# Optimization experiments

Hardware: AMD Instinct MI355X
Metric: run time of the kernel (lower is better)

Reference implementation:

```python
import jax, jax.numpy as jnp
import numpy as np

JACCARD_THRESH = 0.5
NEGPOS_RATIO = 3
V0, V1 = 0.1, 0.2  # SSD encoding variances


def setup_inputs() -> dict:
    key = jax.random.key(0)
    k1, k2, k3, k4, k5, k6, k7 = jax.random.split(key, 7)
    B, P, C, O = 128, 8732, 21, 16
    loc_data = jax.random.normal(k1, (B, P, 4), dtype=jnp.float32)
    conf_data = jax.random.normal(k2, (B, P, C), dtype=jnp.float32)
    # default boxes in center form (cx, cy, w, h), all in [0,1]
    cxcy = jax.random.uniform(k3, (P, 2), minval=0.05, maxval=0.95)
    wh = jax.random.uniform(k4, (P, 2), minval=0.05, maxval=0.6)
    dbox_list = jnp.concatenate([cxcy, wh], axis=1).astype(jnp.float32)
    # ground-truth boxes in corner form with guaranteed positive extent
    tl = jax.random.uniform(k5, (B, O, 2), minval=0.0, maxval=0.6)
    sz = jax.random.uniform(k6, (B, O, 2), minval=0.05, maxval=0.35)
    labels = jax.random.randint(k7, (B, O, 1), 0, C - 1).astype(jnp.float32)
    targets = jnp.concatenate([tl, tl + sz, labels], axis=2)
    return {"loc_data": loc_data, "conf_data": conf_data,
            "dbox_list": dbox_list, "targets": targets}


def _match_one(truths, labels, dbox):
    """SSD match for one image. truths:[O,4] corner, labels:[O], dbox:[P,4] center."""
    pf = jnp.concatenate([dbox[:, :2] - dbox[:, 2:] * 0.5,
                          dbox[:, :2] + dbox[:, 2:] * 0.5], axis=1)  # point form [P,4]
    lt = jnp.maximum(truths[:, None, :2], pf[None, :, :2])
    rb = jnp.minimum(truths[:, None, 2:], pf[None, :, 2:])
    whi = jnp.clip(rb - lt, 0.0)
    inter = whi[..., 0] * whi[..., 1]                                # [O,P]
    area_t = (truths[:, 2] - truths[:, 0]) * (truths[:, 3] - truths[:, 1])
    area_p = dbox[:, 2] * dbox[:, 3]
    ov = inter / (area_t[:, None] + area_p[None, :] - inter)         # jaccard [O,P]
    best_prior_idx = jnp.argmax(ov, axis=1)                          # [O]
    bto = jnp.max(ov, axis=0)                                        # [P]
    bti = jnp.argmax(ov, axis=0)                                     # [P]
    bto = bto.at[best_prior_idx].set(2.0)
    O = truths.shape[0]
    bti = jax.lax.fori_loop(0, O, lambda j, b: b.at[best_prior_idx[j]].set(j), bti)
    matched = truths[bti]                                            # [P,4]
    conf = labels[bti].astype(jnp.int32) + 1
    conf = jnp.where(bto < JACCARD_THRESH, 0, conf)
    g_cxcy = ((matched[:, :2] + matched[:, 2:]) * 0.5 - dbox[:, :2]) / (V0 * dbox[:, 2:])
    g_wh = jnp.log((matched[:, 2:] - matched[:, :2]) / dbox[:, 2:]) / V1
    return jnp.concatenate([g_cxcy, g_wh], axis=1), conf


def reference(loc_data, conf_data, dbox_list, targets):
    B, P, C = conf_data.shape
    loc_t, conf_t = jax.vmap(_match_one, in_axes=(0, 0, None))(
        targets[..., :4], targets[..., 4], dbox_list)
    pos = conf_t > 0                                                  # [B,P]
    # smooth L1 (beta=1), summed over positives
    ad = jnp.abs(loc_data - loc_t)
    sl1 = jnp.where(ad < 1.0, 0.5 * ad * ad, ad - 0.5)
    loss_l = jnp.sum(jnp.where(pos[..., None], sl1, 0.0))
    # per-prior cross entropy
    logp = jax.nn.log_softmax(conf_data, axis=-1)
    ce = -jnp.take_along_axis(logp, conf_t[..., None], axis=-1)[..., 0]  # [B,P]
    # hard negative mining via double argsort (rank in descending order)
    ce_neg = jnp.where(pos, 0.0, ce)
    loss_idx = jnp.argsort(-ce_neg, axis=1)
    idx_rank = jnp.argsort(loss_idx, axis=1)
    num_pos = jnp.sum(pos, axis=1, keepdims=True)
    num_neg = jnp.minimum(num_pos * NEGPOS_RATIO, P)
    neg = idx_rank < num_neg
    sel = pos | neg
    loss_c = jnp.sum(jnp.where(sel, ce, 0.0))
    N = jnp.sum(num_pos).astype(loc_data.dtype)
    return jnp.stack([loss_l / N, loss_c / N])
```

## Files before the change

### kernel.cpp

```cpp
#include <hip/hip_runtime.h>
#include <cstddef>

#define Bn 128
#define Pn 8732
#define Cn 21
#define On 16
#define MAGIC 0x13579BDFu

__device__ __forceinline__ void argmax_combine(float& v, int& p, float v2, int p2) {
  if (v2 > v || (v2 == v && p2 < p)) { v = v2; p = p2; }
}

__device__ __forceinline__ float sl1_enc(float4 lv, float4 d,
                                         float t0, float t1, float t2, float t3) {
  float g0 = ((t0 + t2) * 0.5f - d.x) / (0.1f * d.z);
  float g1 = ((t1 + t3) * 0.5f - d.y) / (0.1f * d.w);
  float g2 = __logf((t2 - t0) / d.z) / 0.2f;
  float g3 = __logf((t3 - t1) / d.w) / 0.2f;
  float r = 0.f, a;
  a = fabsf(lv.x - g0); r += (a < 1.f) ? 0.5f * a * a : a - 0.5f;
  a = fabsf(lv.y - g1); r += (a < 1.f) ? 0.5f * a * a : a - 0.5f;
  a = fabsf(lv.z - g2); r += (a < 1.f) ? 0.5f * a * a : a - 0.5f;
  a = fabsf(lv.w - g3); r += (a < 1.f) ? 0.5f * a * a : a - 0.5f;
  return r;
}

__global__ __launch_bounds__(256) void stream_kernel(
    const float* __restrict__ conf, const float* __restrict__ dbox,
    const float* __restrict__ targets,
    float* __restrict__ ce0, unsigned char* __restrict__ pack,
    unsigned long long* __restrict__ keys) {
  const int wb = threadIdx.x >> 6, lane = threadIdx.x & 63;
  const int wave_g = blockIdx.x * 4 + wb;
  const int b = wave_g & 127;
  const int cg = wave_g >> 7;

  __shared__ float4 s_row4[4][336];
  __shared__ float s_tt[4][On * 5];
  __shared__ float s_ar[4][On];

  for (int i = lane; i < On * 5; i += 64)
    s_tt[wb][i] = targets[(size_t)b * On * 5 + i];
  if (lane < On) {
    float x1 = targets[(size_t)b * On * 5 + lane * 5 + 0];
    float y1 = targets[(size_t)b * On * 5 + lane * 5 + 1];
    float x2 = targets[(size_t)b * On * 5 + lane * 5 + 2];
    float y2 = targets[(size_t)b * On * 5 + lane * 5 + 3];
    s_ar[wb][lane] = (x2 - x1) * (y2 - y1);
  }

  float bestv[On]; int bestp[On];
  #pragma unroll
  for (int j = 0; j < On; j++) { bestv[j] = -1.0f; bestp[j] = 0x7fffffff; }

  #pragma unroll
  for (int i = 0; i < 5; i++) {
    const int ci = cg + 32 * i;
    if (ci >= 137) break;
    const int p0 = ci * 64;
    const int rows = min(64, Pn - p0);
    const int n4 = rows * Cn / 4;

    const float4* src = (const float4*)(conf + ((size_t)b * Pn + p0) * Cn);
    float4 v0, v1, v2, v3, v4, v5;
    if (lane < n4)        v0 = src[lane];
    if (lane + 64 < n4)   v1 = src[lane + 64];
    if (lane + 128 < n4)  v2 = src[lane + 128];
    if (lane + 192 < n4)  v3 = src[lane + 192];
    if (lane + 256 < n4)  v4 = src[lane + 256];
    if (lane + 320 < n4)  v5 = src[lane + 320];
    if (lane < n4)        s_row4[wb][lane] = v0;
    if (lane + 64 < n4)   s_row4[wb][lane + 64] = v1;
    if (lane + 128 < n4)  s_row4[wb][lane + 128] = v2;
    if (lane + 192 < n4)  s_row4[wb][lane + 192] = v3;
    if (lane + 256 < n4)  s_row4[wb][lane + 256] = v4;
    if (lane + 320 < n4)  s_row4[wb][lane + 320] = v5;

    if (lane < rows) {
      const int p = p0 + lane;
      const float* x = (const float*)s_row4[wb] + lane * Cn;
      float g0 = fmaxf(fmaxf(x[0],  x[1]),  x[2]);
      float g1 = fmaxf(fmaxf(x[3],  x[4]),  x[5]);
      float g2 = fmaxf(fmaxf(x[6],  x[7]),  x[8]);
      float g3 = fmaxf(fmaxf(x[9],  x[10]), x[11]);
      float g4 = fmaxf(fmaxf(x[12], x[13]), x[14]);
      float g5 = fmaxf(fmaxf(x[15], x[16]), x[17]);
      float g6 = fmaxf(fmaxf(x[18], x[19]), x[20]);
      float ha = fmaxf(fmaxf(g0, g1), g2);
      float hb = fmaxf(fmaxf(g3, g4), g5);
      float m  = fmaxf(fmaxf(ha, hb), g6);
      float s0 = __expf(x[0] - m), s1 = __expf(x[1] - m);
      float s2 = __expf(x[2] - m), s3 = __expf(x[3] - m);
      #pragma unroll
      for (int q = 4; q < 20; q += 4) {
        s0 += __expf(x[q]     - m);
        s1 += __expf(x[q + 1] - m);
        s2 += __expf(x[q + 2] - m);
        s3 += __expf(x[q + 3] - m);
      }
      s0 += __expf(x[20] - m);
      float s = (s0 + s1) + (s2 + s3);
      float lse = m + __logf(s);
      ce0[(size_t)b * Pn + p] = lse - x[0];

      float4 d = ((const float4*)dbox)[p];
      float px1 = d.x - d.z * 0.5f, py1 = d.y - d.w * 0.5f;
      float px2 = d.x + d.z * 0.5f, py2 = d.y + d.w * 0.5f;
      float ap = d.z * d.w;
      float mv0 = -1.0f, mv1 = -1.0f; int mj0 = 0, mj1 = 8;
      #pragma unroll
      for (int j = 0; j < 8; j++) {
        float lx = fmaxf(s_tt[wb][j*5+0], px1);
        float ly = fmaxf(s_tt[wb][j*5+1], py1);
        float rx = fminf(s_tt[wb][j*5+2], px2);
        float ry = fminf(s_tt[wb][j*5+3], py2);
        float w = fmaxf(rx - lx, 0.0f), h = fmaxf(ry - ly, 0.0f);
        float inter = w * h;
        float ov = __fdividef(inter, s_ar[wb][j] + ap - inter);
        if (ov > bestv[j]) { bestv[j] = ov; bestp[j] = p; }
        if (ov > mv0) { mv0 = ov; mj0 = j; }
      }
      #pragma unroll
      for (int j = 8; j < On; j++) {
        float lx = fmaxf(s_tt[wb][j*5+0], px1);
        float ly = fmaxf(s_tt[wb][j*5+1], py1);
        float rx = fminf(s_tt[wb][j*5+2], px2);
        float ry = fminf(s_tt[wb][j*5+3], py2);
        float w = fmaxf(rx - lx, 0.0f), h = fmaxf(ry - ly, 0.0f);
        float inter = w * h;
        float ov = __fdividef(inter, s_ar[wb][j] + ap - inter);
        if (ov > bestv[j]) { bestv[j] = ov; bestp[j] = p; }
        if (ov > mv1) { mv1 = ov; mj1 = j; }
      }
      float mv; int mj;
      if (mv1 > mv0) { mv = mv1; mj = mj1; } else { mv = mv0; mj = mj0; }
      pack[(size_t)b * Pn + p] =
          (unsigned char)(mj | ((mv >= 0.5f) ? 16 : 0));
    }
  }

  #pragma unroll
  for (int j = 0; j < On; j++) {
    float v = bestv[j]; int p = bestp[j];
    #pragma unroll
    for (int off = 32; off; off >>= 1) {
      float v2 = __shfl_down(v, off);
      int p2 = __shfl_down(p, off);
      argmax_combine(v, p, v2, p2);
    }
    if (lane == 0) {
      unsigned long long key;
      if (v < 0.0f) key = 0xC000000000000000ull;
      else key = (((unsigned long long)(__float_as_uint(v) | 0xC0000000u)) << 32)
               | (unsigned long long)(0xFFFFFFFFu - (unsigned)p);
      atomicMax(&keys[b * On + j], key);
    }
  }
}

__global__ __launch_bounds__(1024) void reduce_kernel(
    const float* __restrict__ loc, const float* __restrict__ conf,
    const float* __restrict__ dbox, const float* __restrict__ targets,
    const float* __restrict__ ce0, const unsigned char* __restrict__ pack,
    const unsigned long long* __restrict__ keys,
    unsigned int* __restrict__ res, float* __restrict__ out) {
  const int b = blockIdx.x;
  const int tid = threadIdx.x;
  const int wave = tid >> 6, lane = tid & 63;

  __shared__ float s_t[On * 5];
  __shared__ int s_bp[On];
  __shared__ unsigned s_bm[273];
  __shared__ unsigned hist[256 * 16];
  __shared__ unsigned s_col[256];
  __shared__ unsigned s_cand[64];
  __shared__ float s_redf[2][16];
  __shared__ int s_redi[16];
  __shared__ unsigned s_prefix;
  __shared__ int s_kk;
  __shared__ int s_cnt;
  __shared__ int s_cc;
  __shared__ int s_np;
  __shared__ float s_floc, s_fcep;

  if (tid < On * 5) s_t[tid] = targets[(size_t)b * On * 5 + tid];
  if (tid < 273) s_bm[tid] = 0;
  __syncthreads();
  if (tid < On) {
    int bp = (int)(0xFFFFFFFFu - (unsigned)(keys[b * On + tid] & 0xFFFFFFFFull));
    s_bp[tid] = bp;
    atomicOr(&s_bm[bp >> 5], 1u << (bp & 31));
  }
  __syncthreads();

  if (wave == 0) {
    float f_loc = 0.f, f_cep = 0.f;
    const bool valid = lane < On;
    const int p = valid ? s_bp[lane] : 0;
    bool dup = false;
    if (valid)
      for (int j2 = lane + 1; j2 < On; j2++) dup |= (s_bp[j2] == p);
    if (valid && !dup) {
      const float* row = conf + ((size_t)b * Pn + p) * Cn;
      float m = row[0];
      #pragma unroll
      for (int q = 1; q < Cn; q++) m = fmaxf(m, row[q]);
      float s = 0.f;
      #pragma unroll
      for (int q = 0; q < Cn; q++) s += __expf(row[q] - m);
      const float lse = m + __logf(s);
      const int c = (int)s_t[lane * 5 + 4] + 1;
      f_cep = lse - row[c];
      const float4 d = ((const float4*)dbox)[p];
      const float4 lv = ((const float4*)loc)[(size_t)b * Pn + p];
      f_loc = sl1_enc(lv, d, s_t[lane*5+0], s_t[lane*5+1],
                             s_t[lane*5+2], s_t[lane*5+3]);
    }
    #pragma unroll
    for (int off = 32; off; off >>= 1) {
      f_loc += __shfl_down(f_loc, off);
      f_cep += __shfl_down(f_cep, off);
    }
    if (lane == 0) { s_floc = f_loc; s_fcep = f_cep; }
  }

  float ce_r[9];
  float my_loc = 0.0f, my_cep = 0.0f; int my_np = 0;
  #pragma unroll
  for (int sI = 0; sI < 9; sI++) {
    ce_r[sI] = 0.0f;
    const int p = tid + 1024 * sI;
    if (p < Pn) {
      unsigned char pk = pack[(size_t)b * Pn + p];
      float c0 = ce0[(size_t)b * Pn + p];
      const unsigned forced = (s_bm[p >> 5] >> (p & 31)) & 1u;
      const int posb = (pk >> 4);
      const int pos = posb | (int)forced;
      ce_r[sI] = pos ? 0.0f : c0;
      if (pos) my_np++;
      if (posb && !forced) {
        const int bt = pk & 15;
        const float* t = &s_t[bt * 5];
        int c = (int)t[4] + 1;
        const float* row = conf + ((size_t)b * Pn + p) * Cn;
        my_cep += c0 + row[0] - row[c];
        float4 d = ((const float4*)dbox)[p];
        float4 ld = ((const float4*)loc)[(size_t)b * Pn + p];
        my_loc += sl1_enc(ld, d, t[0], t[1], t[2], t[3]);
      }
    }
  }

  {
    int np = my_np;
    #pragma unroll
    for (int off = 32; off; off >>= 1) np += __shfl_down(np, off);
    if (lane == 0) s_redi[wave] = np;
  }
  __syncthreads();
  if (tid == 0) {
    int np = 0;
    #pragma unroll
    for (int w = 0; w < 16; w++) np += s_redi[w];
    s_np = np;
  }
  __syncthreads();

  const int k = min(s_np * 3, Pn);
  unsigned prefix = 0, maskb = 0;
  int kk = k;
  int cntc = Pn;
  for (int shift = 24; shift >= 0; shift -= 8) {
    if (cntc <= 64) break;
    ((uint4*)hist)[tid] = make_uint4(0u, 0u, 0u, 0u);
    __syncthreads();
    #pragma unroll
    for (int sI = 0; sI < 9; sI++) {
      const int p = tid + 1024 * sI;
      if (p < Pn) {
        unsigned u = __float_as_uint(ce_r[sI]);
        if ((u & maskb) == prefix)
          atomicAdd(&hist[(((u >> shift) & 255u) << 4) + (unsigned)wave], 1u);
      }
    }
    __syncthreads();
    if (tid < 256) {
      unsigned c = 0;
      #pragma unroll
      for (int w = 0; w < 16; w++) c += hist[(tid << 4) + w];
      s_col[tid] = c;
    }
    __syncthreads();
    if (tid < 64) {
      unsigned c0 = s_col[4 * tid + 0], c1 = s_col[4 * tid + 1];
      unsigned c2 = s_col[4 * tid + 2], c3 = s_col[4 * tid + 3];
      unsigned t0 = c0 + c1 + c2 + c3;
      unsigned S = t0;
      #pragma unroll
      for (int off = 1; off < 64; off <<= 1) {
        unsigned o = __shfl_down(S, off);
        if (tid + off < 64) S += o;
      }
      unsigned Snext = S - t0;
      unsigned s3 = Snext + c3;
      unsigned s2 = s3 + c2;
      unsigned s1 = s2 + c1;
      unsigned s0 = s1 + c0;
      unsigned kk_u = (unsigned)kk;
      int chosen = -1; unsigned snx = 0, cc = 0;
      if (s3 >= kk_u && Snext < kk_u)      { chosen = 3; snx = Snext; cc = c3; }
      else if (s2 >= kk_u && s3 < kk_u)    { chosen = 2; snx = s3;    cc = c2; }
      else if (s1 >= kk_u && s2 < kk_u)    { chosen = 1; snx = s2;    cc = c1; }
      else if (s0 >= kk_u && s1 < kk_u)    { chosen = 0; snx = s1;    cc = c0; }
      if (chosen >= 0) {
        s_prefix = prefix | ((unsigned)(4 * tid + chosen) << shift);
        s_kk = (int)(kk_u - snx);
        s_cnt = (int)cc;
      }
    }
    __syncthreads();
    prefix = s_prefix; kk = s_kk; cntc = s_cnt;
    maskb |= 255u << shift;
  }
  if (maskb != 0xFFFFFFFFu) {
    if (tid == 0) s_cc = 0;
    __syncthreads();
    #pragma unroll
    for (int sI = 0; sI < 9; sI++) {
      const int p = tid + 1024 * sI;
      if (p < Pn) {
        unsigned u = __float_as_uint(ce_r[sI]);
        if ((u & maskb) == prefix) {
          int ix = atomicAdd(&s_cc, 1);
          if (ix < 64) s_cand[ix] = u;
        }
      }
    }
    __syncthreads();
    if (tid < 64) {
      int c = min(s_cc, 64);
      if (tid < c) {
        unsigned v = s_cand[tid];
        int g = 0, e = 0;
        for (int i = 0; i < c; i++) {
          unsigned w = s_cand[i];
          g += (w > v); e += (w == v);
        }
        if (g < kk && kk <= g + e) s_prefix = v;
      }
    }
    __syncthreads();
    prefix = s_prefix;
  }
  float T = __uint_as_float(prefix);

  float sum_gt = 0.0f; int cnt_gt = 0;
  #pragma unroll
  for (int sI = 0; sI < 9; sI++) {
    const int p = tid + 1024 * sI;
    if (p < Pn) {
      float x = ce_r[sI];
      if (x > T) { sum_gt += x; cnt_gt++; }
    }
  }
  #pragma unroll
  for (int off = 32; off; off >>= 1) {
    sum_gt += __shfl_down(sum_gt, off);
    cnt_gt += __shfl_down(cnt_gt, off);
    my_loc += __shfl_down(my_loc, off);
    my_cep += __shfl_down(my_cep, off);
  }
  if (lane == 0) {
    s_redf[0][wave] = my_loc; s_redf[1][wave] = sum_gt + my_cep; s_redi[wave] = cnt_gt;
  }
  __syncthreads();
  if (tid == 0) {
    float ll = s_floc, lc = s_fcep; int cg2 = 0;
    #pragma unroll
    for (int w = 0; w < 16; w++) {
      ll += s_redf[0][w]; lc += s_redf[1][w]; cg2 += s_redi[w];
    }
    lc += (k > 0) ? (float)(k - cg2) * T : 0.0f;
    atomicExch(&res[b * 4 + 0], __float_as_uint(ll));
    atomicExch(&res[b * 4 + 1], __float_as_uint(lc));
    atomicExch(&res[b * 4 + 2], (unsigned)s_np);
    __threadfence();
    atomicExch(&res[b * 4 + 3], MAGIC);
  }

  if (b == 0 && tid < 64) {
    float ll = 0.0f, lc = 0.0f; int np = 0;
    #pragma unroll
    for (int h = 0; h < 2; h++) {
      const int i = tid + 64 * h;
      while (atomicAdd(&res[i * 4 + 3], 0u) != MAGIC) { __builtin_amdgcn_s_sleep(8); }
      ll += __uint_as_float(atomicAdd(&res[i * 4 + 0], 0u));
      lc += __uint_as_float(atomicAdd(&res[i * 4 + 1], 0u));
      np += (int)atomicAdd(&res[i * 4 + 2], 0u);
    }
    #pragma unroll
    for (int off = 32; off; off >>= 1) {
      ll += __shfl_down(ll, off);
      lc += __shfl_down(lc, off);
      np += __shfl_down(np, off);
    }
    if (tid == 0) {
      float fN = (float)np;
      out[0] = ll / fN;
      out[1] = lc / fN;
    }
  }
}

extern "C" void kernel_launch(void* const* d_in, const int* in_sizes, int n_in,
                              void* d_out, int out_size, void* d_ws, size_t ws_size,
                              hipStream_t stream) {
  const float* loc_data  = (const float*)d_in[0];
  const float* conf_data = (const float*)d_in[1];
  const float* dbox      = (const float*)d_in[2];
  const float* targets   = (const float*)d_in[3];
  float* out = (float*)d_out;

  char* ws = (char*)d_ws;
  float* ce0 = (float*)ws;
  unsigned char* pack = (unsigned char*)(ws + (size_t)Bn * Pn * 4);
  unsigned long long* keys =
      (unsigned long long*)(ws + (size_t)Bn * Pn * 5);
  unsigned int* res = (unsigned int*)(ws + (size_t)Bn * Pn * 5 + Bn * On * 8);

  stream_kernel<<<1024, 256, 0, stream>>>(conf_data, dbox, targets, ce0, pack, keys);
  reduce_kernel<<<Bn, 1024, 0, stream>>>(loc_data, conf_data, dbox, targets,
                                         ce0, pack, keys, res, out);
}
```

Before: 200.3 us.

## Fuse stream and reduce kernels using last-arriving-block handoff per image

Merges the streaming match/CE kernel and the per-image reduction kernel into one launch of 256 blocks of 1024 threads. Each image is split across two blocks, and the second block to finish (tracked with an atomic counter) runs the hard-negative selection and reduction. The last block to finish overall computes the final output, replacing the spin-wait on MAGIC flags. The two phases share LDS through a union. This removes a kernel boundary and lets each image's reduction start early, at the cost of an extra memset launch, lower parallelism in the streaming phase (one large block per CU) and only 128 blocks doing the reduction.

```diff
diff --git a/kernel.cpp b/kernel.cpp
--- a/kernel.cpp
+++ b/kernel.cpp
@@ -5,7 +5,6 @@
 #define Pn 8732
 #define Cn 21
 #define On 16
-#define MAGIC 0x13579BDFu
 
 __device__ __forceinline__ void argmax_combine(float& v, int& p, float v2, int p2) {
   if (v2 > v || (v2 == v && p2 < p)) { v = v2; p = p2; }
@@ -25,28 +24,50 @@
   return r;
 }
 
-__global__ __launch_bounds__(256) void stream_kernel(
-    const float* __restrict__ conf, const float* __restrict__ dbox,
-    const float* __restrict__ targets,
+union SmemU {
+  struct {
+    float4 row4[16][336];
+    float  tt[16][On * 5];
+    float  ar[16][On];
+  } st;
+  struct {
+    unsigned hist[256 * 16];
+    unsigned col[256];
+    unsigned cand[64];
+    unsigned bm[273];
+    float    t[On * 5];
+    int      bp[On];
+    float    redf[2][16];
+    int      redi[16];
+  } rd;
+};
+
+__global__ __launch_bounds__(1024) void fused_kernel(
+    const float* __restrict__ loc, const float* __restrict__ conf,
+    const float* __restrict__ dbox, const float* __restrict__ targets,
     float* __restrict__ ce0, unsigned char* __restrict__ pack,
-    unsigned long long* __restrict__ keys) {
-  const int wb = threadIdx.x >> 6, lane = threadIdx.x & 63;
-  const int wave_g = blockIdx.x * 4 + wb;
-  const int b = wave_g & 127;
-  const int cg = wave_g >> 7;
-
-  __shared__ float4 s_row4[4][336];
-  __shared__ float s_tt[4][On * 5];
-  __shared__ float s_ar[4][On];
+    unsigned long long* __restrict__ keys,
+    unsigned* __restrict__ res, unsigned* __restrict__ done,
+    unsigned* __restrict__ done2, float* __restrict__ out) {
+  const int tid = threadIdx.x;
+  const int wb = tid >> 6, lane = tid & 63;
+  const int b = blockIdx.x >> 1;
+  const int cg = (blockIdx.x & 1) * 16 + wb;
+
+  __shared__ SmemU u;
+  __shared__ int s_do, s_fin;
+  __shared__ unsigned s_prefix;
+  __shared__ int s_kk, s_cnt, s_cc, s_np;
+  __shared__ float s_floc, s_fcep;
 
   for (int i = lane; i < On * 5; i += 64)
-    s_tt[wb][i] = targets[(size_t)b * On * 5 + i];
+    u.st.tt[wb][i] = targets[(size_t)b * On * 5 + i];
   if (lane < On) {
     float x1 = targets[(size_t)b * On * 5 + lane * 5 + 0];
     float y1 = targets[(size_t)b * On * 5 + lane * 5 + 1];
     float x2 = targets[(size_t)b * On * 5 + lane * 5 + 2];
     float y2 = targets[(size_t)b * On * 5 + lane * 5 + 3];
-    s_ar[wb][lane] = (x2 - x1) * (y2 - y1);
+    u.st.ar[wb][lane] = (x2 - x1) * (y2 - y1);
   }
 
   float bestv[On]; int bestp[On];
@@ -69,16 +90,16 @@
     if (lane + 192 < n4)  v3 = src[lane + 192];
     if (lane + 256 < n4)  v4 = src[lane + 256];
     if (lane + 320 < n4)  v5 = src[lane + 320];
-    if (lane < n4)        s_row4[wb][lane] = v0;
-    if (lane + 64 < n4)   s_row4[wb][lane + 64] = v1;
-    if (lane + 128 < n4)  s_row4[wb][lane + 128] = v2;
-    if (lane + 192 < n4)  s_row4[wb][lane + 192] = v3;
-    if (lane + 256 < n4)  s_row4[wb][lane + 256] = v4;
-    if (lane + 320 < n4)  s_row4[wb][lane + 320] = v5;
+    if (lane < n4)        u.st.row4[wb][lane] = v0;
+    if (lane + 64 < n4)   u.st.row4[wb][lane + 64] = v1;
+    if (lane + 128 < n4)  u.st.row4[wb][lane + 128] = v2;
+    if (lane + 192 < n4)  u.st.row4[wb][lane + 192] = v3;
+    if (lane + 256 < n4)  u.st.row4[wb][lane + 256] = v4;
+    if (lane + 320 < n4)  u.st.row4[wb][lane + 320] = v5;
 
     if (lane < rows) {
       const int p = p0 + lane;
-      const float* x = (const float*)s_row4[wb] + lane * Cn;
+      const float* x = (const float*)u.st.row4[wb] + lane * Cn;
       float g0 = fmaxf(fmaxf(x[0],  x[1]),  x[2]);
       float g1 = fmaxf(fmaxf(x[3],  x[4]),  x[5]);
       float g2 = fmaxf(fmaxf(x[6],  x[7]),  x[8]);
@@ -86,9 +107,8 @@
       float g4 = fmaxf(fmaxf(x[12], x[13]), x[14]);
       float g5 = fmaxf(fmaxf(x[15], x[16]), x[17]);
       float g6 = fmaxf(fmaxf(x[18], x[19]), x[20]);
-      float ha = fmaxf(fmaxf(g0, g1), g2);
-      float hb = fmaxf(fmaxf(g3, g4), g5);
-      float m  = fmaxf(fmaxf(ha, hb), g6);
+      float m  = fmaxf(fmaxf(fmaxf(fmaxf(g0, g1), g2),
+                             fmaxf(fmaxf(g3, g4), g5)), g6);
       float s0 = __expf(x[0] - m), s1 = __expf(x[1] - m);
       float s2 = __expf(x[2] - m), s3 = __expf(x[3] - m);
       #pragma unroll
@@ -99,8 +119,7 @@
         s3 += __expf(x[q + 3] - m);
       }
       s0 += __expf(x[20] - m);
-      float s = (s0 + s1) + (s2 + s3);
-      float lse = m + __logf(s);
+      float lse = m + __logf((s0 + s1) + (s2 + s3));
       ce0[(size_t)b * Pn + p] = lse - x[0];
 
       float4 d = ((const float4*)dbox)[p];
@@ -110,25 +129,25 @@
       float mv0 = -1.0f, mv1 = -1.0f; int mj0 = 0, mj1 = 8;
       #pragma unroll
       for (int j = 0; j < 8; j++) {
-        float lx = fmaxf(s_tt[wb][j*5+0], px1);
-        float ly = fmaxf(s_tt[wb][j*5+1], py1);
-        float rx = fminf(s_tt[wb][j*5+2], px2);
-        float ry = fminf(s_tt[wb][j*5+3], py2);
+        float lx = fmaxf(u.st.tt[wb][j*5+0], px1);
+        float ly = fmaxf(u.st.tt[wb][j*5+1], py1);
+        float rx = fminf(u.st.tt[wb][j*5+2], px2);
+        float ry = fminf(u.st.tt[wb][j*5+3], py2);
         float w = fmaxf(rx - lx, 0.0f), h = fmaxf(ry - ly, 0.0f);
         float inter = w * h;
-        float ov = __fdividef(inter, s_ar[wb][j] + ap - inter);
+        float ov = __fdividef(inter, u.st.ar[wb][j] + ap - inter);
         if (ov > bestv[j]) { bestv[j] = ov; bestp[j] = p; }
         if (ov > mv0) { mv0 = ov; mj0 = j; }
       }
       #pragma unroll
       for (int j = 8; j < On; j++) {
-        float lx = fmaxf(s_tt[wb][j*5+0], px1);
-        float ly = fmaxf(s_tt[wb][j*5+1], py1);
-        float rx = fminf(s_tt[wb][j*5+2], px2);
-        float ry = fminf(s_tt[wb][j*5+3], py2);
+        float lx = fmaxf(u.st.tt[wb][j*5+0], px1);
+        float ly = fmaxf(u.st.tt[wb][j*5+1], py1);
+        float rx = fminf(u.st.tt[wb][j*5+2], px2);
+        float ry = fminf(u.st.tt[wb][j*5+3], py2);
         float w = fmaxf(rx - lx, 0.0f), h = fmaxf(ry - ly, 0.0f);
         float inter = w * h;
-        float ov = __fdividef(inter, s_ar[wb][j] + ap - inter);
+        float ov = __fdividef(inter, u.st.ar[wb][j] + ap - inter);
         if (ov > bestv[j]) { bestv[j] = ov; bestp[j] = p; }
         if (ov > mv1) { mv1 = ov; mj1 = j; }
       }
@@ -156,50 +175,34 @@
       atomicMax(&keys[b * On + j], key);
     }
   }
-}
-
-__global__ __launch_bounds__(1024) void reduce_kernel(
-    const float* __restrict__ loc, const float* __restrict__ conf,
-    const float* __restrict__ dbox, const float* __restrict__ targets,
-    const float* __restrict__ ce0, const unsigned char* __restrict__ pack,
-    const unsigned long long* __restrict__ keys,
-    unsigned int* __restrict__ res, float* __restrict__ out) {
-  const int b = blockIdx.x;
-  const int tid = threadIdx.x;
-  const int wave = tid >> 6, lane = tid & 63;
-
-  __shared__ float s_t[On * 5];
-  __shared__ int s_bp[On];
-  __shared__ unsigned s_bm[273];
-  __shared__ unsigned hist[256 * 16];
-  __shared__ unsigned s_col[256];
-  __shared__ unsigned s_cand[64];
-  __shared__ float s_redf[2][16];
-  __shared__ int s_redi[16];
-  __shared__ unsigned s_prefix;
-  __shared__ int s_kk;
-  __shared__ int s_cnt;
-  __shared__ int s_cc;
-  __shared__ int s_np;
-  __shared__ float s_floc, s_fcep;
-
-  if (tid < On * 5) s_t[tid] = targets[(size_t)b * On * 5 + tid];
-  if (tid < 273) s_bm[tid] = 0;
+
+  __syncthreads();
+  if (tid == 0) {
+    __threadfence();
+    unsigned o = atomicAdd(&done[b], 1u);
+    s_do = (o == 1u) ? 1 : 0;
+  }
+  __syncthreads();
+  if (!s_do) return;
+  __threadfence();
+
+  if (tid < On * 5) u.rd.t[tid] = targets[(size_t)b * On * 5 + tid];
+  if (tid < 273) u.rd.bm[tid] = 0;
   __syncthreads();
   if (tid < On) {
     int bp = (int)(0xFFFFFFFFu - (unsigned)(keys[b * On + tid] & 0xFFFFFFFFull));
-    s_bp[tid] = bp;
-    atomicOr(&s_bm[bp >> 5], 1u << (bp & 31));
-  }
-  __syncthreads();
-
-  if (wave == 0) {
+    u.rd.bp[tid] = bp;
+    atomicOr(&u.rd.bm[bp >> 5], 1u << (bp & 31));
+  }
+  __syncthreads();
+
+  if (wb == 0) {
     float f_loc = 0.f, f_cep = 0.f;
     const bool valid = lane < On;
-    const int p = valid ? s_bp[lane] : 0;
+    const int p = valid ? u.rd.bp[lane] : 0;
     bool dup = false;
     if (valid)
-      for (int j2 = lane + 1; j2 < On; j2++) dup |= (s_bp[j2] == p);
+      for (int j2 = lane + 1; j2 < On; j2++) dup |= (u.rd.bp[j2] == p);
     if (valid && !dup) {
       const float* row = conf + ((size_t)b * Pn + p) * Cn;
       float m = row[0];
@@ -209,12 +212,12 @@
       #pragma unroll
       for (int q = 0; q < Cn; q++) s += __expf(row[q] - m);
       const float lse = m + __logf(s);
-      const int c = (int)s_t[lane * 5 + 4] + 1;
+      const int c = (int)u.rd.t[lane * 5 + 4] + 1;
       f_cep = lse - row[c];
       const float4 d = ((const float4*)dbox)[p];
       const float4 lv = ((const float4*)loc)[(size_t)b * Pn + p];
-      f_loc = sl1_enc(lv, d, s_t[lane*5+0], s_t[lane*5+1],
-                             s_t[lane*5+2], s_t[lane*5+3]);
+      f_loc = sl1_enc(lv, d, u.rd.t[lane*5+0], u.rd.t[lane*5+1],
+                             u.rd.t[lane*5+2], u.rd.t[lane*5+3]);
     }
     #pragma unroll
     for (int off = 32; off; off >>= 1) {
@@ -233,14 +236,14 @@
     if (p < Pn) {
       unsigned char pk = pack[(size_t)b * Pn + p];
       float c0 = ce0[(size_t)b * Pn + p];
-      const unsigned forced = (s_bm[p >> 5] >> (p & 31)) & 1u;
+      const unsigned forced = (u.rd.bm[p >> 5] >> (p & 31)) & 1u;
       const int posb = (pk >> 4);
       const int pos = posb | (int)forced;
       ce_r[sI] = pos ? 0.0f : c0;
       if (pos) my_np++;
       if (posb && !forced) {
         const int bt = pk & 15;
-        const float* t = &s_t[bt * 5];
+        const float* t = &u.rd.t[bt * 5];
         int c = (int)t[4] + 1;
         const float* row = conf + ((size_t)b * Pn + p) * Cn;
         my_cep += c0 + row[0] - row[c];
@@ -255,13 +258,13 @@
     int np = my_np;
     #pragma unroll
     for (int off = 32; off; off >>= 1) np += __shfl_down(np, off);
-    if (lane == 0) s_redi[wave] = np;
+    if (lane == 0) u.rd.redi[wb] = np;
   }
   __syncthreads();
   if (tid == 0) {
     int np = 0;
     #pragma unroll
-    for (int w = 0; w < 16; w++) np += s_redi[w];
+    for (int w = 0; w < 16; w++) np += u.rd.redi[w];
     s_np = np;
   }
   __syncthreads();
@@ -272,28 +275,28 @@
   int cntc = Pn;
   for (int shift = 24; shift >= 0; shift -= 8) {
     if (cntc <= 64) break;
-    ((uint4*)hist)[tid] = make_uint4(0u, 0u, 0u, 0u);
+    ((uint4*)u.rd.hist)[tid] = make_uint4(0u, 0u, 0u, 0u);
     __syncthreads();
     #pragma unroll
     for (int sI = 0; sI < 9; sI++) {
       const int p = tid + 1024 * sI;
       if (p < Pn) {
-        unsigned u = __float_as_uint(ce_r[sI]);
-        if ((u & maskb) == prefix)
-          atomicAdd(&hist[(((u >> shift) & 255u) << 4) + (unsigned)wave], 1u);
+        unsigned uu = __float_as_uint(ce_r[sI]);
+        if ((uu & maskb) == prefix)
+          atomicAdd(&u.rd.hist[(((uu >> shift) & 255u) << 4) + (unsigned)wb], 1u);
       }
     }
     __syncthreads();
     if (tid < 256) {
       unsigned c = 0;
       #pragma unroll
-      for (int w = 0; w < 16; w++) c += hist[(tid << 4) + w];
-      s_col[tid] = c;
+      for (int w = 0; w < 16; w++) c += u.rd.hist[(tid << 4) + w];
+      u.rd.col[tid] = c;
     }
     __syncthreads();
     if (tid < 64) {
-      unsigned c0 = s_col[4 * tid + 0], c1 = s_col[4 * tid + 1];
-      unsigned c2 = s_col[4 * tid + 2], c3 = s_col[4 * tid + 3];
+      unsigned c0 = u.rd.col[4 * tid + 0], c1 = u.rd.col[4 * tid + 1];
+      unsigned c2 = u.rd.col[4 * tid + 2], c3 = u.rd.col[4 * tid + 3];
       unsigned t0 = c0 + c1 + c2 + c3;
       unsigned S = t0;
       #pragma unroll
@@ -329,10 +332,10 @@
     for (int sI = 0; sI < 9; sI++) {
       const int p = tid + 1024 * sI;
       if (p < Pn) {
-        unsigned u = __float_as_uint(ce_r[sI]);
-        if ((u & maskb) == prefix) {
+        unsigned uu = __float_as_uint(ce_r[sI]);
+        if ((uu & maskb) == prefix) {
           int ix = atomicAdd(&s_cc, 1);
-          if (ix < 64) s_cand[ix] = u;
+          if (ix < 64) u.rd.cand[ix] = uu;
         }
       }
     }
@@ -340,10 +343,10 @@
     if (tid < 64) {
       int c = min(s_cc, 64);
       if (tid < c) {
-        unsigned v = s_cand[tid];
+        unsigned v = u.rd.cand[tid];
         int g = 0, e = 0;
         for (int i = 0; i < c; i++) {
-          unsigned w = s_cand[i];
+          unsigned w = u.rd.cand[i];
           g += (w > v); e += (w == v);
         }
         if (g < kk && kk <= g + e) s_prefix = v;
@@ -371,32 +374,34 @@
     my_cep += __shfl_down(my_cep, off);
   }
   if (lane == 0) {
-    s_redf[0][wave] = my_loc; s_redf[1][wave] = sum_gt + my_cep; s_redi[wave] = cnt_gt;
+    u.rd.redf[0][wb] = my_loc;
+    u.rd.redf[1][wb] = sum_gt + my_cep;
+    u.rd.redi[wb] = cnt_gt;
   }
   __syncthreads();
   if (tid == 0) {
     float ll = s_floc, lc = s_fcep; int cg2 = 0;
     #pragma unroll
     for (int w = 0; w < 16; w++) {
-      ll += s_redf[0][w]; lc += s_redf[1][w]; cg2 += s_redi[w];
+      ll += u.rd.redf[0][w]; lc += u.rd.redf[1][w]; cg2 += u.rd.redi[w];
     }
     lc += (k > 0) ? (float)(k - cg2) * T : 0.0f;
     atomicExch(&res[b * 4 + 0], __float_as_uint(ll));
     atomicExch(&res[b * 4 + 1], __float_as_uint(lc));
     atomicExch(&res[b * 4 + 2], (unsigned)s_np);
     __threadfence();
-    atomicExch(&res[b * 4 + 3], MAGIC);
-  }
-
-  if (b == 0 && tid < 64) {
+    unsigned o2 = atomicAdd(done2, 1u);
+    s_fin = (o2 == (unsigned)(Bn - 1)) ? 1 : 0;
+  }
+  __syncthreads();
+
+  if (s_fin) {
+    __threadfence();
     float ll = 0.0f, lc = 0.0f; int np = 0;
-    #pragma unroll
-    for (int h = 0; h < 2; h++) {
-      const int i = tid + 64 * h;
-      while (atomicAdd(&res[i * 4 + 3], 0u) != MAGIC) { __builtin_amdgcn_s_sleep(8); }
-      ll += __uint_as_float(atomicAdd(&res[i * 4 + 0], 0u));
-      lc += __uint_as_float(atomicAdd(&res[i * 4 + 1], 0u));
-      np += (int)atomicAdd(&res[i * 4 + 2], 0u);
+    if (tid < Bn) {
+      ll = __uint_as_float(atomicAdd(&res[tid * 4 + 0], 0u));
+      lc = __uint_as_float(atomicAdd(&res[tid * 4 + 1], 0u));
+      np = (int)atomicAdd(&res[tid * 4 + 2], 0u);
     }
     #pragma unroll
     for (int off = 32; off; off >>= 1) {
@@ -404,10 +409,16 @@
       lc += __shfl_down(lc, off);
       np += __shfl_down(np, off);
     }
+    if (lane == 0 && wb < 2) {
+      u.rd.redf[0][wb] = ll; u.rd.redf[1][wb] = lc; u.rd.redi[wb] = np;
+    }
+    __syncthreads();
     if (tid == 0) {
-      float fN = (float)np;
-      out[0] = ll / fN;
-      out[1] = lc / fN;
+      float L = u.rd.redf[0][0] + u.rd.redf[0][1];
+      float C = u.rd.redf[1][0] + u.rd.redf[1][1];
+      float N = (float)(u.rd.redi[0] + u.rd.redi[1]);
+      out[0] = L / N;
+      out[1] = C / N;
     }
   }
 }
@@ -426,9 +437,13 @@
   unsigned char* pack = (unsigned char*)(ws + (size_t)Bn * Pn * 4);
   unsigned long long* keys =
       (unsigned long long*)(ws + (size_t)Bn * Pn * 5);
-  unsigned int* res = (unsigned int*)(ws + (size_t)Bn * Pn * 5 + Bn * On * 8);
-
-  stream_kernel<<<1024, 256, 0, stream>>>(conf_data, dbox, targets, ce0, pack, keys);
-  reduce_kernel<<<Bn, 1024, 0, stream>>>(loc_data, conf_data, dbox, targets,
-                                         ce0, pack, keys, res, out);
+  unsigned int* res =
+      (unsigned int*)(ws + (size_t)Bn * Pn * 5 + (size_t)Bn * On * 8);
+  unsigned int* done  = res + Bn * 4;
+  unsigned int* done2 = done + Bn;
+
+  hipMemsetAsync(done, 0, (size_t)(Bn + 1) * sizeof(unsigned), stream);
+
+  fused_kernel<<<2 * Bn, 1024, 0, stream>>>(
+      loc_data, conf_data, dbox, targets, ce0, pack, keys, res, done, done2, out);
 }
```

Measured after the change: 260.3 us. 30.0% more time.
